# Optimization experiments

Measured on AMD Instinct MI355X. Metric: run time of the kernel, lower is better.

Reference implementation:

```python
import jax, jax.numpy as jnp
import numpy as np

NUM_QUERIES = 256
NUM_NEGATIVES = 512
NUM_GENERALIZED = 8
GEN_RADIUS = 1.0
TEMP = 0.5
STRONG_THRESHOLD = 0.97


def _mls(mu0, mu1, s0, s1):
    # mutual likelihood score; mu's are L2-normalized (F.normalize, eps=1e-12)
    mu0 = mu0 / jnp.maximum(jnp.linalg.norm(mu0, axis=-1, keepdims=True), 1e-12)
    mu1 = mu1 / jnp.maximum(jnp.linalg.norm(mu1, axis=-1, keepdims=True), 1e-12)
    down = s0 + s1
    return -0.5 * (((mu0 - mu1) ** 2) / down + jnp.log(down)).mean(-1)


def setup_inputs() -> dict:
    key = jax.random.key(0)
    B, S, H, W, C = 4, 19, 128, 128, 256
    ks = jax.random.split(key, 6)
    mu = jax.random.normal(ks[0], (B, C, H, W), jnp.float32)
    sigma = jax.random.uniform(ks[1], (B, C, H, W), jnp.float32, minval=0.1, maxval=1.0)
    cls = jax.random.randint(ks[2], (B, H, W), 0, S)
    label = jnp.transpose(jax.nn.one_hot(cls, S, dtype=jnp.float32), (0, 3, 1, 2))  # [B,S,H,W]
    mask = jnp.ones((B, 1, H, W), jnp.float32)
    prob = jax.random.uniform(ks[3], (B, S, H, W), jnp.float32)
    mmt_prototype_mu = jax.random.normal(ks[4], (S, 1, C), jnp.float32)
    mmt_prototype_sigma = jax.random.uniform(ks[5], (S, 1, C), jnp.float32, minval=0.1, maxval=1.0)
    return {"mu": mu, "sigma": sigma, "label": label, "mask": mask, "prob": prob,
            "mmt_prototype_mu": mmt_prototype_mu, "mmt_prototype_sigma": mmt_prototype_sigma,
            "epoch": 0, "iter_i": 0}


def reference(mu, sigma, label, mask, prob, mmt_prototype_mu, mmt_prototype_sigma, epoch, iter_i):
    B, C, H, W = mu.shape
    S = label.shape[1]
    P = B * H * W
    Q, NEG, G = NUM_QUERIES, NUM_NEGATIVES, NUM_GENERALIZED
    key = jax.random.key(1234)

    valid = (label * mask).transpose(1, 0, 2, 3).reshape(S, P)            # [S,P] float
    mu_f = mu.transpose(0, 2, 3, 1).reshape(P, C)                          # [P,C]
    sg_f = sigma.transpose(0, 2, 3, 1).reshape(P, C)
    prob_f = prob.transpose(1, 0, 2, 3).reshape(S, P)
    hard = (prob_f < STRONG_THRESHOLD).astype(valid.dtype) * valid         # [S,P]

    # --- segment prototypes (precision-weighted fusion), detached as in torch.no_grad ---
    inv_sg = 1.0 / sg_f
    proto_sigma_b = 1.0 / jnp.einsum('sp,pc->sc', valid, inv_sg)           # [S,C]
    proto_mu_b = proto_sigma_b * jnp.einsum('sp,pc->sc', valid, inv_sg * mu_f)
    mmt_mu = mmt_prototype_mu[:, 0, :]
    mmt_sg = mmt_prototype_sigma[:, 0, :]
    proto_sigma = 1.0 / (1.0 / proto_sigma_b + 1.0 / mmt_sg)               # momentum fusion
    proto_mu = proto_sigma * (mmt_mu / mmt_sg + proto_mu_b / proto_sigma_b)
    proto_mu = jax.lax.stop_gradient(proto_mu)
    proto_sigma = jax.lax.stop_gradient(proto_sigma)

    # cumulative masks for uniform sampling over valid / hard pixels via searchsorted
    valid_cum = jnp.cumsum(valid, axis=1)                                  # [S,P]
    valid_cnt = valid_cum[:, -1]
    hard_cum = jnp.cumsum(hard, axis=1)
    hard_cnt = hard_cum[:, -1]

    loss = jnp.float32(0.0)
    for i in range(S):
        ki = jax.random.fold_in(key, i)
        k_anc, k_cls, k_neg, k_gen = jax.random.split(ki, 4)
        # anchors: uniform over hard pixels of segment i
        u = jax.random.uniform(k_anc, (Q,)) * hard_cnt[i]
        a_idx = jnp.clip(jnp.searchsorted(hard_cum[i], u, side='right'), 0, P - 1)
        anchor_mu = mu_f[a_idx]                                            # [Q,C]
        anchor_sg = sg_f[a_idx]
        # negative class distribution from prototype MLS similarity
        others = jnp.concatenate([jnp.arange(i + 1, S), jnp.arange(0, i)])  # [S-1]
        sim = _mls(proto_mu[i][None], proto_mu[others], proto_sigma[i][None], proto_sigma[others])
        logp = jax.nn.log_softmax(sim / TEMP)
        samp = jax.random.categorical(k_cls, logp, shape=(Q, NEG))          # idx into `others`
        cls_g = others[samp.reshape(-1)]                                    # [Q*NEG] global class
        # uniform pixel within each sampled class (vectorized searchsorted over classes)
        un = jax.random.uniform(k_neg, (Q * NEG,))
        idx_all = jax.vmap(lambda cs, cnt: jnp.searchsorted(cs, un * cnt, side='right'))(valid_cum, valid_cnt)
        n_idx = jnp.clip(idx_all[cls_g, jnp.arange(Q * NEG)], 0, P - 1)
        neg_mu = jax.lax.stop_gradient(mu_f[n_idx].reshape(Q, NEG, C))
        neg_sg = jax.lax.stop_gradient(sg_f[n_idx].reshape(Q, NEG, C))
        pos_mu = jnp.broadcast_to(proto_mu[i][None, None], (Q, 1, C))
        pos_sg = jnp.broadcast_to(proto_sigma[i][None, None], (Q, 1, C))
        # generalized negatives: reparameterized samples from (updated) momentum prototypes
        eps = jax.random.normal(k_gen, (S - 1, G, C))
        gen = proto_mu[others][:, None, :] + GEN_RADIUS * jnp.sqrt(proto_sigma[others])[:, None, :] * eps
        gen = jnp.broadcast_to(gen.reshape(1, (S - 1) * G, C), (Q, (S - 1) * G, C))
        all_mu = jnp.concatenate([pos_mu, neg_mu, gen], axis=1)             # [Q,1+NEG+(S-1)*G,C]
        all_sg = jnp.concatenate([pos_sg, neg_sg, jnp.zeros_like(gen)], axis=1)
        logits = _mls(anchor_mu[:, None, :], all_mu, anchor_sg[:, None, :], all_sg) / TEMP
        loss = loss - jax.nn.log_softmax(logits, axis=-1)[:, 0].mean()      # CE vs target 0
    return loss / S
```

## Files before the change

### kernel.cpp

```cpp
#include <hip/hip_runtime.h>
#include <hip/hip_fp16.h>
#include <hip/hip_fp8.h>
#include <cstdint>

#define B_   4
#define S_   19
#define HW_  16384
#define P_   65536
#define C_   256
#define Q_   256
#define NEG_ 512
#define NS_  131072
#define GENV_ 144
#define NANCH (S_ * Q_)
#define NPAIR (NANCH / 2)
#define NBUCK 8

typedef float v2f __attribute__((ext_vector_type(2)));

#if __has_builtin(__builtin_amdgcn_cvt_pk_f32_fp8) && __has_builtin(__builtin_amdgcn_cvt_pk_fp8_f32)
#define HAVE_HW_FP8 1
#endif

template<int W> __device__ __forceinline__ v2f cvt8(uint32_t d) {
#ifdef HAVE_HW_FP8
  v2f r = __builtin_amdgcn_cvt_pk_f32_fp8((int)d, W);
  return r;
#else
  __hip_fp8_e4m3 h0, h1;
  h0.__x = (uint8_t)(d >> (W * 16));
  h1.__x = (uint8_t)(d >> (W * 16 + 8));
  v2f r; r.x = (float)h0; r.y = (float)h1; return r;
#endif
}
template<int W> __device__ __forceinline__ uint32_t pk8(float a, float b, uint32_t old) {
#ifdef HAVE_HW_FP8
  return (uint32_t)__builtin_amdgcn_cvt_pk_fp8_f32(a, b, (int)old, W);
#else
  __hip_fp8_e4m3 ha(a), hb(b);
  uint32_t v = (uint32_t)ha.__x | ((uint32_t)hb.__x << 8);
  return (old & (W ? 0x0000FFFFu : 0xFFFF0000u)) | (v << (W * 16));
#endif
}

__device__ __forceinline__ void tf2x32(uint32_t k0, uint32_t k1, uint32_t x0, uint32_t x1,
                                       uint32_t& o0, uint32_t& o1) {
  uint32_t k2 = k0 ^ k1 ^ 0x1BD11BDAu;
#define TFR(r) { x0 += x1; x1 = (x1 << r) | (x1 >> (32 - r)); x1 ^= x0; }
  x0 += k0; x1 += k1;
  TFR(13) TFR(15) TFR(26) TFR(6)  x0 += k1; x1 += k2 + 1u;
  TFR(17) TFR(29) TFR(16) TFR(24) x0 += k2; x1 += k0 + 2u;
  TFR(13) TFR(15) TFR(26) TFR(6)  x0 += k0; x1 += k1 + 3u;
  TFR(17) TFR(29) TFR(16) TFR(24) x0 += k1; x1 += k2 + 4u;
  TFR(13) TFR(15) TFR(26) TFR(6)  x0 += k2; x1 += k0 + 5u;
#undef TFR
  o0 = x0; o1 = x1;
}

__device__ __forceinline__ uint32_t rbits(uint32_t k0, uint32_t k1, uint32_t n) {
  uint32_t a, b; tf2x32(k0, k1, 0u, n, a, b); return a ^ b;
}

__device__ __forceinline__ float bits2f01(uint32_t b) {
  return __uint_as_float((b >> 9) | 0x3f800000u) - 1.0f;
}

__device__ __forceinline__ float fastrcp(float x) {
  float r; asm("v_rcp_f32 %0, %1" : "=v"(r) : "v"(x)); return r;
}

__device__ __forceinline__ float wred(float v) {
#pragma unroll
  for (int off = 32; off > 0; off >>= 1) v += __shfl_xor(v, off, 64);
  return v;
}
__device__ __forceinline__ void wred3(float& a, float& b, float& c) {
#pragma unroll
  for (int off = 32; off > 0; off >>= 1) {
    a += __shfl_xor(a, off, 64);
    b += __shfl_xor(b, off, 64);
    c += __shfl_xor(c, off, 64);
  }
}

__device__ __forceinline__ void lse_up(float lg, float& m, float& l) {
  if (lg > m) { l = l * __expf(m - lg) + 1.0f; m = lg; }
  else l += __expf(lg - m);
}
__device__ __forceinline__ void lse_merge(float& m, float& l, float mo, float lo) {
  float mn = fmaxf(m, mo);
  l = l * __expf(m - mn) + lo * __expf(mo - mn);
  m = mn;
}

__device__ __forceinline__ float erfinv_f(float x) {
  float w = -__logf(fmaxf(fmaf(-x, x, 1.0f), 1e-37f));
  float p;
  if (w < 5.0f) {
    w -= 2.5f;
    p = 2.81022636e-08f;
    p = fmaf(p, w, 3.43273939e-07f);
    p = fmaf(p, w, -3.5233877e-06f);
    p = fmaf(p, w, -4.39150654e-06f);
    p = fmaf(p, w, 0.00021858087f);
    p = fmaf(p, w, -0.00125372503f);
    p = fmaf(p, w, -0.00417768164f);
    p = fmaf(p, w, 0.246640727f);
    p = fmaf(p, w, 1.50140941f);
  } else {
    w = sqrtf(w) - 3.0f;
    p = -0.000200214257f;
    p = fmaf(p, w, 0.000100950558f);
    p = fmaf(p, w, 0.00134934322f);
    p = fmaf(p, w, -0.00367342844f);
    p = fmaf(p, w, 0.00573950773f);
    p = fmaf(p, w, -0.0076224613f);
    p = fmaf(p, w, 0.00943887047f);
    p = fmaf(p, w, 1.00167406f);
    p = fmaf(p, w, 2.83297682f);
  }
  return p * x;
}

__global__ void k_keys(uint32_t* __restrict__ keys) {
  int i = threadIdx.x;
  if (i >= S_) return;
  uint32_t f0, f1;
  tf2x32(0u, 1234u, 0u, (uint32_t)i, f0, f1);
#pragma unroll
  for (int t = 0; t < 4; ++t) {
    uint32_t a, b;
    tf2x32(f0, f1, 0u, (uint32_t)t, a, b);
    keys[i * 8 + t * 2] = a; keys[i * 8 + t * 2 + 1] = b;
  }
}

__global__ __launch_bounds__(256) void k_classify(const float* __restrict__ label,
    const float* __restrict__ mask, const float* __restrict__ prob,
    int* __restrict__ cls, int* __restrict__ hrd) {
  int p = blockIdx.x * 256 + threadIdx.x;
  int b = p >> 14, rem = p & (HW_ - 1);
  int sp = -1;
#pragma unroll
  for (int s = 0; s < S_; ++s) {
    float l = label[((b * S_ + s) << 14) + rem];
    if (l > 0.5f) sp = s;
  }
  if (mask[(b << 14) + rem] <= 0.5f) sp = -1;
  int h = 0;
  if (sp >= 0) h = (prob[((b * S_ + sp) << 14) + rem] < 0.97f) ? 1 : 0;
  cls[p] = sp; hrd[p] = h;
}

__global__ __launch_bounds__(256) void k_pack(const float* __restrict__ mu,
    const float* __restrict__ sg, uint32_t* __restrict__ pair8, float* __restrict__ norm2) {
  __shared__ float smu[64][65];
  __shared__ float ssg[64][65];
  int p0 = blockIdx.x * 64, c0 = blockIdx.y * 64;
  int b = p0 >> 14, rem0 = p0 & (HW_ - 1);
  int px = threadIdx.x & 63, cy = threadIdx.x >> 6;
#pragma unroll
  for (int itr = 0; itr < 16; ++itr) {
    int cl = cy + itr * 4;
    int addr = ((b * C_ + c0 + cl) << 14) + rem0 + px;
    smu[cl][px] = mu[addr];
    ssg[cl][px] = sg[addr];
  }
  __syncthreads();
#pragma unroll
  for (int itr = 0; itr < 8; ++itr) {
    int e = itr * 256 + threadIdx.x;
    int pxl = e >> 5, dw = e & 31, cl = dw * 2;
    uint32_t wd = pk8<0>(smu[cl][pxl], ssg[cl][pxl], 0u);
    wd = pk8<1>(smu[cl + 1][pxl], ssg[cl + 1][pxl], wd);
    pair8[(size_t)(p0 + pxl) * 128 + (c0 >> 1) + dw] = wd;
  }
  int pxn = threadIdx.x >> 2, qn = threadIdx.x & 3;
  float s2 = 0.f;
#pragma unroll
  for (int k = 0; k < 16; ++k) { float v = smu[qn * 16 + k][pxn]; s2 = fmaf(v, v, s2); }
  s2 += __shfl_xor(s2, 1, 64);
  s2 += __shfl_xor(s2, 2, 64);
  if (qn == 0) atomicAdd(&norm2[p0 + pxn], s2);
}

__global__ __launch_bounds__(256) void k_count(const int* __restrict__ cls, const int* __restrict__ hrd,
    int* __restrict__ bcv, int* __restrict__ bch) {
  __shared__ int hv[S_], hh[S_];
  int t = threadIdx.x;
  if (t < S_) { hv[t] = 0; hh[t] = 0; }
  __syncthreads();
  int p = blockIdx.x * 256 + t;
  int s = cls[p];
  if (s >= 0) { atomicAdd(&hv[s], 1); if (hrd[p]) atomicAdd(&hh[s], 1); }
  __syncthreads();
  if (t < S_) { bcv[t * 256 + blockIdx.x] = hv[t]; bch[t * 256 + blockIdx.x] = hh[t]; }
}

__global__ __launch_bounds__(320) void k_scan(const int* __restrict__ bcv, const int* __restrict__ bch,
    int* __restrict__ bov, int* __restrict__ boh,
    int* __restrict__ cntv, int* __restrict__ cnth,
    int* __restrict__ basev, int* __restrict__ baseh) {
  __shared__ int psv[S_][16], psh[S_][16], scv[S_], sch[S_];
  int t = threadIdx.x;
  int s = t >> 4, c = t & 15;
  if (t < 304) {
    int sv = 0, sh = 0;
#pragma unroll 4
    for (int b = 0; b < 16; ++b) {
      sv += bcv[s * 256 + c * 16 + b];
      sh += bch[s * 256 + c * 16 + b];
    }
    psv[s][c] = sv; psh[s][c] = sh;
  }
  __syncthreads();
  if (t < S_) {
    int rv = 0, rh = 0;
#pragma unroll
    for (int cc = 0; cc < 16; ++cc) {
      int tv = psv[t][cc]; psv[t][cc] = rv; rv += tv;
      int th = psh[t][cc]; psh[t][cc] = rh; rh += th;
    }
    cntv[t] = rv; cnth[t] = rh; scv[t] = rv; sch[t] = rh;
  }
  __syncthreads();
  if (t == 0) {
    int bv = 0, bh = 0;
    for (int k = 0; k < S_; ++k) { basev[k] = bv; bv += scv[k]; baseh[k] = bh; bh += sch[k]; }
  }
  if (t < 304) {
    int rv = psv[s][c], rh = psh[s][c];
#pragma unroll 4
    for (int b = 0; b < 16; ++b) {
      int i0 = s * 256 + c * 16 + b;
      int tv = bcv[i0]; bov[i0] = rv; rv += tv;
      int th = bch[i0]; boh[i0] = rh; rh += th;
    }
  }
}

__global__ __launch_bounds__(256) void k_fill(const int* __restrict__ cls, const int* __restrict__ hrd,
    const int* __restrict__ bov, const int* __restrict__ boh,
    const int* __restrict__ basev, const int* __restrict__ baseh,
    int* __restrict__ posv, int* __restrict__ posh) {
  __shared__ int lc[256], lh[256];
  int t = threadIdx.x;
  int p = blockIdx.x * 256 + t;
  int s = cls[p]; int h = hrd[p];
  lc[t] = s; lh[t] = h;
  __syncthreads();
  if (s >= 0) {
    int rv = 0, rh = 0;
    for (int k = 0; k < t; ++k) { if (lc[k] == s) { rv++; rh += lh[k]; } }
    posv[basev[s] + bov[s * 256 + blockIdx.x] + rv] = p;
    if (h) posh[baseh[s] + boh[s * 256 + blockIdx.x] + rh] = p;
  }
}

__global__ __launch_bounds__(256) void k_sums(const uint32_t* __restrict__ pair8,
    const int* __restrict__ cls, float* __restrict__ part) {
  __shared__ float lacc[S_][2][C_];
  __shared__ int scls[256];
  int t = threadIdx.x;
  for (int e = t; e < S_ * 2 * C_; e += 256) (&lacc[0][0][0])[e] = 0.f;
  int p0 = blockIdx.x * 256;
  scls[t] = cls[p0 + t];
  __syncthreads();
  int half = t & 1, dwi = t >> 1;
  uint32_t d = pair8[(size_t)p0 * 128 + dwi];
  for (int pp = 0; pp < 256; ++pp) {
    uint32_t dnx = (pp + 1 < 256) ? pair8[(size_t)(p0 + pp + 1) * 128 + dwi] : 0u;
    int s = scls[pp];
    if (s >= 0) {
      v2f e = half ? cvt8<1>(d) : cvt8<0>(d);
      float ia = fastrcp(e.y);
      lacc[s][0][t] += ia;
      lacc[s][1][t] += ia * e.x;
    }
    d = dnx;
  }
  __syncthreads();
  float* dst = part + (size_t)blockIdx.x * (2 * S_ * C_);
  for (int e = t; e < S_ * 2 * C_; e += 256) dst[e] = (&lacc[0][0][0])[e];
}

__global__ __launch_bounds__(256) void k_proto(const float* __restrict__ part,
    const float* __restrict__ mmu, const float* __restrict__ msg,
    float* __restrict__ pmu, float* __restrict__ psig, float* __restrict__ phat) {
  int s = blockIdx.x, c = threadIdx.x;
  float A = 0.f, Bv = 0.f;
  for (int b = 0; b < 256; ++b) {
    const float* pb = part + (size_t)b * (2 * S_ * C_) + (s * 2) * C_;
    A += pb[c];
    Bv += pb[C_ + c];
  }
  int e = s * C_ + c;
  float psb = 1.0f / A;
  float pmb = psb * Bv;
  float ms = msg[e], mm = mmu[e];
  float ps = 1.0f / (1.0f / psb + 1.0f / ms);
  float pm = ps * (mm / ms + pmb / psb);
  pmu[e] = pm; psig[e] = ps;
  __shared__ float red[4];
  float w = wred(pm * pm);
  int lane = c & 63, wv = c >> 6;
  if (lane == 0) red[wv] = w;
  __syncthreads();
  float tot = red[0] + red[1] + red[2] + red[3];
  float nrm = fmaxf(sqrtf(tot), 1e-12f);
  phat[e] = pm / nrm;
}

__global__ __launch_bounds__(64) void k_simlogp(const float* __restrict__ phat,
    const float* __restrict__ psig, float* __restrict__ logp) {
  int i = blockIdx.x, lane = threadIdx.x;
  int c0 = lane * 4;
  float phi[4], psi[4];
#pragma unroll
  for (int k = 0; k < 4; ++k) { phi[k] = phat[i * C_ + c0 + k]; psi[k] = psig[i * C_ + c0 + k]; }
  float xs[18];
#pragma unroll
  for (int j = 0; j < 18; ++j) {
    int o = i + 1 + j; if (o >= S_) o -= S_;
    float t = 0.f;
#pragma unroll
    for (int k = 0; k < 4; ++k) {
      float d = phi[k] - phat[o * C_ + c0 + k];
      float dn = psi[k] + psig[o * C_ + c0 + k];
      t += d * d / dn + logf(dn);
    }
    t = wred(t);
    xs[j] = (-0.5f * t * (1.0f / 256.0f)) * 2.0f;
  }
  float m = xs[0];
#pragma unroll
  for (int j = 1; j < 18; ++j) m = fmaxf(m, xs[j]);
  float se = 0.f;
#pragma unroll
  for (int j = 0; j < 18; ++j) se += expf(xs[j] - m);
  float lg = logf(se);
  if (lane == 0) {
#pragma unroll
    for (int j = 0; j < 18; ++j) logp[i * 18 + j] = xs[j] - m - lg;
  }
}

__global__ __launch_bounds__(256) void k_anchors(const uint32_t* __restrict__ keys,
    const int* __restrict__ cnth, const int* __restrict__ baseh,
    const int* __restrict__ posh, int* __restrict__ aidx) {
  int i = blockIdx.x, q = threadIdx.x;
  uint32_t k0 = keys[i * 8 + 0], k1 = keys[i * 8 + 1];
  float u = bits2f01(rbits(k0, k1, (uint32_t)q));
  int cnt = cnth[i];
  int idx = P_ - 1;
  if (cnt > 0) {
    int kk = (int)(u * (float)cnt);
    if (kk >= cnt) kk = cnt - 1;
    idx = posh[baseh[i] + kk];
  }
  aidx[i * Q_ + q] = idx;
}

__global__ __launch_bounds__(256) void k_gen(const uint32_t* __restrict__ keys,
    const float* __restrict__ pmu, const float* __restrict__ psig, float* __restrict__ ghat) {
  int v = blockIdx.x, i = blockIdx.y, c = threadIdx.x;
  int o = i + 1 + (v >> 3); if (o >= S_) o -= S_;
  uint32_t k0 = keys[i * 8 + 6], k1 = keys[i * 8 + 7];
  uint32_t bits = rbits(k0, k1, (uint32_t)(v * C_ + c));
  float f01 = bits2f01(bits);
  const float lo = -0.99999994f;
  float u = fmaxf(f01 * 2.0f + lo, lo);
  float eps = 1.41421356237f * erfinv_f(u);
  float g = pmu[o * C_ + c] + sqrtf(psig[o * C_ + c]) * eps;
  __shared__ float red[4];
  float w = wred(g * g);
  int lane = c & 63, wv = c >> 6;
  if (lane == 0) red[wv] = w;
  __syncthreads();
  float tot = red[0] + red[1] + red[2] + red[3];
  float nrm = fmaxf(sqrtf(tot), 1e-12f);
  ghat[((size_t)(i * GENV_ + v)) * C_ + c] = g / nrm;
}

__global__ __launch_bounds__(256) void k_sample(const uint32_t* __restrict__ keys,
    const float* __restrict__ logp, const int* __restrict__ cntv, const int* __restrict__ basev,
    const int* __restrict__ posv, int* __restrict__ nidx) {
  int i = blockIdx.y;
  int m = blockIdx.x * 256 + threadIdx.x;
  __shared__ float lp[18];
  __shared__ int lcnt[S_], lbase[S_];
  int t = threadIdx.x;
  if (t < 18) lp[t] = logp[i * 18 + t];
  if (t < S_) { lcnt[t] = cntv[t]; lbase[t] = basev[t]; }
  __syncthreads();
  uint32_t kc0 = keys[i * 8 + 2], kc1 = keys[i * 8 + 3];
  uint32_t kn0 = keys[i * 8 + 4], kn1 = keys[i * 8 + 5];
  float bv = -1e30f; int best = 0;
  for (int s = 0; s < 18; ++s) {
    uint32_t b = rbits(kc0, kc1, (uint32_t)m * 18u + (uint32_t)s);
    float u = fmaxf(bits2f01(b), 1.17549435e-38f);
    float g = -__logf(-__logf(u)) + lp[s];
    if (g > bv) { bv = g; best = s; }
  }
  float un = bits2f01(rbits(kn0, kn1, (uint32_t)m));
  int cc = i + 1 + best; if (cc >= S_) cc -= S_;
  int cnt = lcnt[cc];
  int idx = P_ - 1;
  if (cnt > 0) {
    int kk = (int)(un * (float)cnt);
    if (kk >= cnt) kk = cnt - 1;
    idx = posv[lbase[cc] + kk];
  }
  nidx[(size_t)i * NS_ + m] = idx;
}

__global__ __launch_bounds__(64) void k_bucket(const int* __restrict__ nidx,
    int* __restrict__ snidx, int* __restrict__ boff) {
  int a = blockIdx.x;
  int lane = threadIdx.x;
  const int* src = nidx + (size_t)a * NEG_;
  int e[8], bk[8];
#pragma unroll
  for (int c = 0; c < 8; ++c) { e[c] = src[c * 64 + lane]; bk[c] = (e[c] >> 13) & 7; }
  uint32_t cnt[NBUCK];
#pragma unroll
  for (int b = 0; b < NBUCK; ++b) cnt[b] = 0;
#pragma unroll
  for (int c = 0; c < 8; ++c)
#pragma unroll
    for (int b = 0; b < NBUCK; ++b) {
      unsigned long long mb = __ballot(bk[c] == b);
      cnt[b] += (uint32_t)__popcll(mb);
    }
  uint32_t base[NBUCK]; uint32_t run = 0;
#pragma unroll
  for (int b = 0; b < NBUCK; ++b) { base[b] = run; run += cnt[b]; }
  if (lane < NBUCK) boff[a * 9 + lane] = (int)base[lane];
  if (lane == 0) boff[a * 9 + 8] = NEG_;
  uint32_t off[NBUCK];
#pragma unroll
  for (int b = 0; b < NBUCK; ++b) off[b] = 0;
  unsigned long long ltm = (1ull << lane) - 1ull;
#pragma unroll
  for (int c = 0; c < 8; ++c) {
    int pos = 0;
#pragma unroll
    for (int b = 0; b < NBUCK; ++b) {
      unsigned long long mb = __ballot(bk[c] == b);
      if (bk[c] == b) pos = (int)(base[b] + off[b] + (uint32_t)__popcll(mb & ltm));
      off[b] += (uint32_t)__popcll(mb);
    }
    snidx[(size_t)a * NEG_ + pos] = e[c];
  }
}

__global__ __launch_bounds__(64) void k_neg(const uint32_t* __restrict__ pair8,
    const float* __restrict__ norm2, const int* __restrict__ snidx,
    const int* __restrict__ boff, const int* __restrict__ aidx,
    float2* __restrict__ partial) {
  __shared__ float4 anc[260];
  __shared__ float4 ah2s[130];
  int bid = blockIdx.x;
  int bucket = bid & 7;
  int pr = bid >> 3;
  int a0 = pr * 2, a1 = a0 + 1;
  int lane = threadIdx.x;

  int ap0 = aidx[a0], ap1 = aidx[a1];
  float rn0 = fastrcp(fmaxf(sqrtf(norm2[ap0]), 1e-12f));
  float rn1 = fastrcp(fmaxf(sqrtf(norm2[ap1]), 1e-12f));
  uint2 d0 = ((const uint2*)(pair8 + (size_t)ap0 * 128))[lane];
  uint2 d1 = ((const uint2*)(pair8 + (size_t)ap1 * 128))[lane];
  {
    v2f ex = cvt8<0>(d0.x), ey = cvt8<1>(d0.x), ez = cvt8<0>(d0.y), ew = cvt8<1>(d0.y);
    float h0 = ex.x * rn0, h1 = ey.x * rn0, h2 = ez.x * rn0, h3 = ew.x * rn0;
    anc[lane * 2]     = make_float4(h0, ex.y, h1, ey.y);
    anc[lane * 2 + 1] = make_float4(h2, ez.y, h3, ew.y);
    ah2s[lane]        = make_float4(h0 * h0, h1 * h1, h2 * h2, h3 * h3);
    ex = cvt8<0>(d1.x); ey = cvt8<1>(d1.x); ez = cvt8<0>(d1.y); ew = cvt8<1>(d1.y);
    h0 = ex.x * rn1; h1 = ey.x * rn1; h2 = ez.x * rn1; h3 = ew.x * rn1;
    anc[130 + lane * 2]     = make_float4(h0, ex.y, h1, ey.y);
    anc[130 + lane * 2 + 1] = make_float4(h2, ez.y, h3, ew.y);
    ah2s[65 + lane]         = make_float4(h0 * h0, h1 * h1, h2 * h2, h3 * h3);
  }
  __syncthreads();

  int s0 = boff[a0 * 9 + bucket], e0i = boff[a0 * 9 + bucket + 1];
  int s1 = boff[a1 * 9 + bucket], e1i = boff[a1 * 9 + bucket + 1];
  int L0 = e0i - s0, L1 = e1i - s1, Lt = L0 + L1;
  const int* list0 = snidx + (size_t)a0 * NEG_ + s0;
  const int* list1 = snidx + (size_t)a1 * NEG_ + s1;

  float m0 = -1e30f, l0 = 0.f, m1 = -1e30f, l1 = 0.f;

  for (int r = 0; r * 64 < Lt; ++r) {
    int g = r * 64 + lane;
    bool act = g < Lt;
    int which = (act && g >= L0) ? 1 : 0;
    int j = which ? (g - L0) : g;
    int p = act ? (which ? list1[j] : list0[j]) : ap0;
    float rnN = fastrcp(fmaxf(sqrtf(norm2[p]), 1e-12f));
    const uint4* rp = (const uint4*)(pair8 + (size_t)p * 128);
    const float4* A = anc + which * 130;
    const float4* H = ah2s + which * 65;
    float sA = 0.f, sC = 0.f, sNR = 0.f, sL = 0.f;
    uint4 c0 = rp[0], c1 = rp[1];
#pragma unroll 1
    for (int it = 0; it < 16; ++it) {
      int nx = ((it + 1) & 15) * 2;
      uint4 n0 = rp[nx], n1 = rp[nx + 1];
      uint32_t dws[8] = {c0.x, c0.y, c0.z, c0.w, c1.x, c1.y, c1.z, c1.w};
      float pp = 1.0f, pq = 1.0f;
#pragma unroll
      for (int gq = 0; gq < 4; ++gq) {
        float4 acA = A[it * 8 + gq * 2];
        float4 acB = A[it * 8 + gq * 2 + 1];
        float4 hh = H[it * 4 + gq];
        v2f e0v = cvt8<0>(dws[2 * gq]),     e1v = cvt8<1>(dws[2 * gq]);
        v2f e2v = cvt8<0>(dws[2 * gq + 1]), e3v = cvt8<1>(dws[2 * gq + 1]);
        float dn0 = acA.y + e0v.y, dn1 = acA.w + e1v.y;
        float dn2 = acB.y + e2v.y, dn3 = acB.w + e3v.y;
        float d01 = dn0 * dn1, d23 = dn2 * dn3;
        float R01 = fastrcp(d01), R23 = fastrcp(d23);
        pp *= d01; pq *= d23;
        float r0 = dn1 * R01, r1 = dn0 * R01, r2 = dn3 * R23, r3 = dn2 * R23;
        sA = fmaf(hh.x, r0, sA); sA = fmaf(hh.y, r1, sA);
        sA = fmaf(hh.z, r2, sA); sA = fmaf(hh.w, r3, sA);
        float q0 = e0v.x * r0; sC = fmaf(acA.x, q0, sC); sNR = fmaf(e0v.x, q0, sNR);
        float q1 = e1v.x * r1; sC = fmaf(acA.z, q1, sC); sNR = fmaf(e1v.x, q1, sNR);
        float q2 = e2v.x * r2; sC = fmaf(acB.x, q2, sC); sNR = fmaf(e2v.x, q2, sNR);
        float q3 = e3v.x * r3; sC = fmaf(acB.z, q3, sC); sNR = fmaf(e3v.x, q3, sNR);
      }
      sL += __logf(pp * pq);
      c0 = n0; c1 = n1;
    }
    float tt = sA + rnN * rnN * sNR - 2.0f * rnN * sC + sL;
    float lg = -tt * (1.0f / 256.0f);
    if (act) { if (which) lse_up(lg, m1, l1); else lse_up(lg, m0, l0); }
  }
#pragma unroll
  for (int o = 32; o > 0; o >>= 1) {
    float mo = __shfl_xor(m0, o, 64), lo = __shfl_xor(l0, o, 64);
    lse_merge(m0, l0, mo, lo);
    mo = __shfl_xor(m1, o, 64); lo = __shfl_xor(l1, o, 64);
    lse_merge(m1, l1, mo, lo);
  }
  if (lane == 0) {
    partial[a0 * NBUCK + bucket] = make_float2(m0, l0);
    partial[a1 * NBUCK + bucket] = make_float2(m1, l1);
  }
}

__global__ __launch_bounds__(256, 4) void k_fin(const uint32_t* __restrict__ pair8,
    const float* __restrict__ norm2,
    const float* __restrict__ phat, const float* __restrict__ psig,
    const float* __restrict__ ghat, const int* __restrict__ aidx,
    const float2* __restrict__ partial, float* __restrict__ out) {
  __shared__ float2 ancG[C_];
  __shared__ float redm[3][4];
  __shared__ float2 mlw[4];

  int bid = blockIdx.x;
  int i = bid >> 8;
  int t = threadIdx.x, w = t >> 6, lane = t & 63;

  int ap = aidx[bid];
  uint32_t ad = pair8[(size_t)ap * 128 + (t >> 1)];
  v2f ae0 = cvt8<0>(ad), ae1 = cvt8<1>(ad);
  float amu = (t & 1) ? ae1.x : ae0.x;
  float asg = (t & 1) ? ae1.y : ae0.y;
  float rn = fastrcp(fmaxf(sqrtf(norm2[ap]), 1e-12f));
  float ahat = amu * rn;
  float wv = fastrcp(asg);
  ancG[t] = make_float2(wv, ahat * wv);

  float pm = phat[i * C_ + t];
  float ps = psig[i * C_ + t];
  float dnp = asg + ps;
  float dd = ahat - pm;
  float post = fmaf(dd * dd, fastrcp(dnp), __logf(dnp));
  float a1t = ahat * ahat * wv;
  float lat = __logf(asg);
  wred3(post, a1t, lat);
  if (lane == 0) { redm[0][w] = post; redm[1][w] = a1t; redm[2][w] = lat; }
  __syncthreads();
  float postS = redm[0][0] + redm[0][1] + redm[0][2] + redm[0][3];
  float Kc = (redm[1][0] + redm[1][1] + redm[1][2] + redm[1][3])
           + (redm[2][0] + redm[2][1] + redm[2][2] + redm[2][3]);
  float logit0 = -postS * (1.0f / 256.0f);

  float m = -1e30f, l = 0.0f;
  const float4* ancGf = (const float4*)ancG;
  if (lane < 36) {
    int g = lane * 4 + w;
    const float4* gp = (const float4*)(ghat + ((size_t)(i * GENV_ + g)) * C_);
    float a1 = 0.f, a2 = 0.f;
    for (int itr = 0; itr < 64; ++itr) {
      float4 gv = gp[itr];
      float4 g01 = ancGf[itr * 2];
      float4 g23 = ancGf[itr * 2 + 1];
      a1 = fmaf(gv.x * gv.x, g01.x, a1); a2 = fmaf(gv.x, g01.y, a2);
      a1 = fmaf(gv.y * gv.y, g01.z, a1); a2 = fmaf(gv.y, g01.w, a2);
      a1 = fmaf(gv.z * gv.z, g23.x, a1); a2 = fmaf(gv.z, g23.y, a2);
      a1 = fmaf(gv.w * gv.w, g23.z, a1); a2 = fmaf(gv.w, g23.w, a2);
    }
    float lg = -(Kc + a1 - 2.0f * a2) * (1.0f / 256.0f);
    lse_up(lg, m, l);
  }
#pragma unroll
  for (int o = 32; o > 0; o >>= 1) {
    float mo = __shfl_xor(m, o, 64);
    float lo = __shfl_xor(l, o, 64);
    lse_merge(m, l, mo, lo);
  }
  if (lane == 0) mlw[w] = make_float2(m, l);
  __syncthreads();
  if (t == 0) {
    float mm = mlw[0].x, ll = mlw[0].y;
    lse_merge(mm, ll, mlw[1].x, mlw[1].y);
    lse_merge(mm, ll, mlw[2].x, mlw[2].y);
    lse_merge(mm, ll, mlw[3].x, mlw[3].y);
    const float2* pp = partial + (size_t)bid * NBUCK;
#pragma unroll
    for (int b = 0; b < NBUCK; ++b) lse_merge(mm, ll, pp[b].x, pp[b].y);
    lse_merge(mm, ll, logit0, 1.0f);
    float lse = mm + __logf(ll);
    float contrib = logit0 - lse;
    atomicAdd(out, -contrib * (1.0f / (19.0f * 256.0f)));
  }
}

extern "C" void kernel_launch(void* const* d_in, const int* in_sizes, int n_in,
                              void* d_out, int out_size, void* d_ws, size_t ws_size,
                              hipStream_t stream) {
  const float* mu    = (const float*)d_in[0];
  const float* sg    = (const float*)d_in[1];
  const float* label = (const float*)d_in[2];
  const float* mask  = (const float*)d_in[3];
  const float* prob  = (const float*)d_in[4];
  const float* mmu   = (const float*)d_in[5];
  const float* msg   = (const float*)d_in[6];

  char* ws = (char*)d_ws;
  size_t off = 0;
  auto take = [&](size_t bytes) { size_t r = off; off = (off + bytes + 255) & ~(size_t)255; return r; };
  size_t o_pair8 = take((size_t)P_ * 128 * 4);
  size_t o_norm2 = take((size_t)P_ * 4);
  size_t o_cls   = take((size_t)P_ * 4);
  size_t o_hrd   = take((size_t)P_ * 4);
  size_t o_bcv   = take(S_ * 256 * 4);
  size_t o_bch   = take(S_ * 256 * 4);
  size_t o_bov   = take(S_ * 256 * 4);
  size_t o_boh   = take(S_ * 256 * 4);
  size_t o_cntv  = take(S_ * 4);
  size_t o_cnth  = take(S_ * 4);
  size_t o_basev = take(S_ * 4);
  size_t o_baseh = take(S_ * 4);
  size_t o_posv  = take((size_t)P_ * 4);
  size_t o_posh  = take((size_t)P_ * 4);
  size_t o_part  = take((size_t)256 * 2 * S_ * C_ * 4);
  size_t o_pmu   = take(S_ * C_ * 4);
  size_t o_psig  = take(S_ * C_ * 4);
  size_t o_phat  = take(S_ * C_ * 4);
  size_t o_logp  = take(S_ * 18 * 4);
  size_t o_keys  = take(S_ * 8 * 4);
  size_t o_aidx  = take(S_ * Q_ * 4);
  size_t o_nidx  = take((size_t)S_ * NS_ * 4);
  size_t o_snidx = take((size_t)S_ * NS_ * 4);
  size_t o_boff  = take((size_t)NANCH * 9 * 4);
  size_t o_lpar  = take((size_t)NANCH * NBUCK * 8);
  size_t o_ghat  = take((size_t)S_ * GENV_ * C_ * 4);
  if (ws_size < off) return;

  uint32_t* pair8 = (uint32_t*)(ws + o_pair8);
  float*    norm2 = (float*)(ws + o_norm2);
  int*      cls   = (int*)(ws + o_cls);
  int*      hrd   = (int*)(ws + o_hrd);
  int*      bcv   = (int*)(ws + o_bcv);
  int*      bch   = (int*)(ws + o_bch);
  int*      bov   = (int*)(ws + o_bov);
  int*      boh   = (int*)(ws + o_boh);
  int*      cntv  = (int*)(ws + o_cntv);
  int*      cnth  = (int*)(ws + o_cnth);
  int*      basev = (int*)(ws + o_basev);
  int*      baseh = (int*)(ws + o_baseh);
  int*      posv  = (int*)(ws + o_posv);
  int*      posh  = (int*)(ws + o_posh);
  float*    part  = (float*)(ws + o_part);
  float*    pmu   = (float*)(ws + o_pmu);
  float*    psig  = (float*)(ws + o_psig);
  float*    phat  = (float*)(ws + o_phat);
  float*    logp  = (float*)(ws + o_logp);
  uint32_t* keys  = (uint32_t*)(ws + o_keys);
  int*      aidx  = (int*)(ws + o_aidx);
  int*      nidx  = (int*)(ws + o_nidx);
  int*      snidx = (int*)(ws + o_snidx);
  int*      boff  = (int*)(ws + o_boff);
  float2*   lpar  = (float2*)(ws + o_lpar);
  float*    ghat  = (float*)(ws + o_ghat);

  hipMemsetAsync(ws + o_norm2, 0, (size_t)P_ * 4, stream);
  hipMemsetAsync(d_out, 0, (size_t)out_size * 4, stream);

  k_keys<<<1, 64, 0, stream>>>(keys);
  k_classify<<<256, 256, 0, stream>>>(label, mask, prob, cls, hrd);
  k_pack<<<dim3(P_ / 64, C_ / 64), 256, 0, stream>>>(mu, sg, pair8, norm2);
  k_count<<<256, 256, 0, stream>>>(cls, hrd, bcv, bch);
  k_scan<<<1, 320, 0, stream>>>(bcv, bch, bov, boh, cntv, cnth, basev, baseh);
  k_fill<<<256, 256, 0, stream>>>(cls, hrd, bov, boh, basev, baseh, posv, posh);
  k_sums<<<256, 256, 0, stream>>>(pair8, cls, part);
  k_proto<<<S_, 256, 0, stream>>>(part, mmu, msg, pmu, psig, phat);
  k_simlogp<<<S_, 64, 0, stream>>>(phat, psig, logp);
  k_anchors<<<S_, 256, 0, stream>>>(keys, cnth, baseh, posh, aidx);
  k_gen<<<dim3(GENV_, S_), 256, 0, stream>>>(keys, pmu, psig, ghat);
  k_sample<<<dim3(512, S_), 256, 0, stream>>>(keys, logp, cntv, basev, posv, nidx);
  k_bucket<<<NANCH, 64, 0, stream>>>(nidx, snidx, boff);
  k_neg<<<NBUCK * NPAIR, 64, 0, stream>>>(pair8, norm2, snidx, boff, aidx, lpar);
  k_fin<<<NANCH, 256, 0, stream>>>(pair8, norm2, phat, psig, ghat, aidx, lpar, (float*)d_out);
}
```

Before: 657.9 us.

## Split fp8 pair rows into separate mu and sigma halves for packed math

Changes the packed fp8 row layout from interleaved (mu,sigma) pairs to a mu half followed by a sigma half, so each dword holds four channels of one quantity. k_neg keeps the anchor in three separate shared arrays and does the per-channel MLS math with 2-wide vector ops (a macro), aiming for packed FP32 instructions and fewer conversions per dword. k_pack switches to float4 global loads, and k_sums/k_fin are updated to the new layout. The risk is more shared-memory reads per iteration, and k_sums loses its software prefetch.

```diff
diff --git a/kernel.cpp b/kernel.cpp
--- a/kernel.cpp
+++ b/kernel.cpp
@@ -12,7 +12,7 @@
 #define NEG_ 512
 #define NS_  131072
 #define GENV_ 144
-#define NANCH (S_ * Q_)
+#define NANCH (S_ * 256)
 #define NPAIR (NANCH / 2)
 #define NBUCK 8
 
@@ -158,22 +158,31 @@
   __shared__ float ssg[64][65];
   int p0 = blockIdx.x * 64, c0 = blockIdx.y * 64;
   int b = p0 >> 14, rem0 = p0 & (HW_ - 1);
-  int px = threadIdx.x & 63, cy = threadIdx.x >> 6;
-#pragma unroll
-  for (int itr = 0; itr < 16; ++itr) {
-    int cl = cy + itr * 4;
-    int addr = ((b * C_ + c0 + cl) << 14) + rem0 + px;
-    smu[cl][px] = mu[addr];
-    ssg[cl][px] = sg[addr];
-  }
-  __syncthreads();
-#pragma unroll
-  for (int itr = 0; itr < 8; ++itr) {
+  int cl0 = threadIdx.x >> 4, px4 = (threadIdx.x & 15) * 4;
+#pragma unroll
+  for (int itr = 0; itr < 4; ++itr) {
+    int cl = cl0 + itr * 16;
+    int addr = ((b * C_ + c0 + cl) << 14) + rem0 + px4;
+    float4 vm = *reinterpret_cast<const float4*>(mu + addr);
+    float4 vs = *reinterpret_cast<const float4*>(sg + addr);
+    smu[cl][px4 + 0] = vm.x; smu[cl][px4 + 1] = vm.y;
+    smu[cl][px4 + 2] = vm.z; smu[cl][px4 + 3] = vm.w;
+    ssg[cl][px4 + 0] = vs.x; ssg[cl][px4 + 1] = vs.y;
+    ssg[cl][px4 + 2] = vs.z; ssg[cl][px4 + 3] = vs.w;
+  }
+  __syncthreads();
+#pragma unroll
+  for (int itr = 0; itr < 4; ++itr) {
     int e = itr * 256 + threadIdx.x;
-    int pxl = e >> 5, dw = e & 31, cl = dw * 2;
-    uint32_t wd = pk8<0>(smu[cl][pxl], ssg[cl][pxl], 0u);
-    wd = pk8<1>(smu[cl + 1][pxl], ssg[cl + 1][pxl], wd);
-    pair8[(size_t)(p0 + pxl) * 128 + (c0 >> 1) + dw] = wd;
+    int pxl = e >> 4, dq = e & 15;
+    int cb = dq * 4;
+    uint32_t wm = pk8<0>(smu[cb][pxl], smu[cb + 1][pxl], 0u);
+    wm = pk8<1>(smu[cb + 2][pxl], smu[cb + 3][pxl], wm);
+    uint32_t wsv = pk8<0>(ssg[cb][pxl], ssg[cb + 1][pxl], 0u);
+    wsv = pk8<1>(ssg[cb + 2][pxl], ssg[cb + 3][pxl], wsv);
+    size_t rowb = (size_t)(p0 + pxl) * 128;
+    pair8[rowb + (c0 >> 2) + dq] = wm;
+    pair8[rowb + 64 + (c0 >> 2) + dq] = wsv;
   }
   int pxn = threadIdx.x >> 2, qn = threadIdx.x & 3;
   float s2 = 0.f;
@@ -266,18 +275,21 @@
   int p0 = blockIdx.x * 256;
   scls[t] = cls[p0 + t];
   __syncthreads();
-  int half = t & 1, dwi = t >> 1;
-  uint32_t d = pair8[(size_t)p0 * 128 + dwi];
+  int dq = t >> 2, sub = t & 3;
   for (int pp = 0; pp < 256; ++pp) {
-    uint32_t dnx = (pp + 1 < 256) ? pair8[(size_t)(p0 + pp + 1) * 128 + dwi] : 0u;
     int s = scls[pp];
+    size_t rowb = (size_t)(p0 + pp) * 128;
+    uint32_t dm = pair8[rowb + dq];
+    uint32_t dsv = pair8[rowb + 64 + dq];
     if (s >= 0) {
-      v2f e = half ? cvt8<1>(d) : cvt8<0>(d);
-      float ia = fastrcp(e.y);
+      v2f em = (sub & 2) ? cvt8<1>(dm) : cvt8<0>(dm);
+      v2f es = (sub & 2) ? cvt8<1>(dsv) : cvt8<0>(dsv);
+      float mv = (sub & 1) ? em.y : em.x;
+      float sv = (sub & 1) ? es.y : es.x;
+      float ia = fastrcp(sv);
       lacc[s][0][t] += ia;
-      lacc[s][1][t] += ia * e.x;
-    }
-    d = dnx;
+      lacc[s][1][t] += ia * mv;
+    }
   }
   __syncthreads();
   float* dst = part + (size_t)blockIdx.x * (2 * S_ * C_);
@@ -454,12 +466,35 @@
   }
 }
 
+#define PKQ(DM, DS, QI) {                                         \
+    float4 ah4 = AH[QI]; float4 as4 = AS[QI]; float4 h24 = H2[QI];\
+    v2f m01 = cvt8<0>(DM), m23 = cvt8<1>(DM);                     \
+    v2f g01 = cvt8<0>(DS), g23 = cvt8<1>(DS);                     \
+    v2f asA; asA.x = as4.x; asA.y = as4.y;                        \
+    v2f asB; asB.x = as4.z; asB.y = as4.w;                        \
+    v2f dA = asA + g01;                                           \
+    v2f dB = asB + g23;                                           \
+    float dpA = dA.x * dA.y, dpB = dB.x * dB.y;                   \
+    float RA = fastrcp(dpA), RB = fastrcp(dpB);                   \
+    pp *= dpA * dpB;                                              \
+    v2f rA; rA.x = dA.y * RA; rA.y = dA.x * RA;                   \
+    v2f rB; rB.x = dB.y * RB; rB.y = dB.x * RB;                   \
+    v2f h2A; h2A.x = h24.x; h2A.y = h24.y;                        \
+    v2f h2B; h2B.x = h24.z; h2B.y = h24.w;                        \
+    sAv += h2A * rA; sAv += h2B * rB;                             \
+    v2f qA = m01 * rA, qB = m23 * rB;                             \
+    v2f ahA; ahA.x = ah4.x; ahA.y = ah4.y;                        \
+    v2f ahB; ahB.x = ah4.z; ahB.y = ah4.w;                        \
+    sCv += ahA * qA; sCv += ahB * qB;                             \
+    sNRv += m01 * qA; sNRv += m23 * qB; }
+
 __global__ __launch_bounds__(64) void k_neg(const uint32_t* __restrict__ pair8,
     const float* __restrict__ norm2, const int* __restrict__ snidx,
     const int* __restrict__ boff, const int* __restrict__ aidx,
     float2* __restrict__ partial) {
-  __shared__ float4 anc[260];
-  __shared__ float4 ah2s[130];
+  __shared__ float4 ahP[2][66];
+  __shared__ float4 asP[2][66];
+  __shared__ float4 h2P[2][66];
   int bid = blockIdx.x;
   int bucket = bid & 7;
   int pr = bid >> 3;
@@ -469,19 +504,23 @@
   int ap0 = aidx[a0], ap1 = aidx[a1];
   float rn0 = fastrcp(fmaxf(sqrtf(norm2[ap0]), 1e-12f));
   float rn1 = fastrcp(fmaxf(sqrtf(norm2[ap1]), 1e-12f));
-  uint2 d0 = ((const uint2*)(pair8 + (size_t)ap0 * 128))[lane];
-  uint2 d1 = ((const uint2*)(pair8 + (size_t)ap1 * 128))[lane];
   {
-    v2f ex = cvt8<0>(d0.x), ey = cvt8<1>(d0.x), ez = cvt8<0>(d0.y), ew = cvt8<1>(d0.y);
-    float h0 = ex.x * rn0, h1 = ey.x * rn0, h2 = ez.x * rn0, h3 = ew.x * rn0;
-    anc[lane * 2]     = make_float4(h0, ex.y, h1, ey.y);
-    anc[lane * 2 + 1] = make_float4(h2, ez.y, h3, ew.y);
-    ah2s[lane]        = make_float4(h0 * h0, h1 * h1, h2 * h2, h3 * h3);
-    ex = cvt8<0>(d1.x); ey = cvt8<1>(d1.x); ez = cvt8<0>(d1.y); ew = cvt8<1>(d1.y);
-    h0 = ex.x * rn1; h1 = ey.x * rn1; h2 = ez.x * rn1; h3 = ew.x * rn1;
-    anc[130 + lane * 2]     = make_float4(h0, ex.y, h1, ey.y);
-    anc[130 + lane * 2 + 1] = make_float4(h2, ez.y, h3, ew.y);
-    ah2s[65 + lane]         = make_float4(h0 * h0, h1 * h1, h2 * h2, h3 * h3);
+    const uint32_t* r0 = pair8 + (size_t)ap0 * 128;
+    uint32_t dm = r0[lane], dsv = r0[64 + lane];
+    v2f m01 = cvt8<0>(dm), m23 = cvt8<1>(dm);
+    v2f s01 = cvt8<0>(dsv), s23 = cvt8<1>(dsv);
+    float h0 = m01.x * rn0, h1 = m01.y * rn0, h2 = m23.x * rn0, h3 = m23.y * rn0;
+    ahP[0][lane] = make_float4(h0, h1, h2, h3);
+    asP[0][lane] = make_float4(s01.x, s01.y, s23.x, s23.y);
+    h2P[0][lane] = make_float4(h0 * h0, h1 * h1, h2 * h2, h3 * h3);
+    const uint32_t* r1 = pair8 + (size_t)ap1 * 128;
+    dm = r1[lane]; dsv = r1[64 + lane];
+    m01 = cvt8<0>(dm); m23 = cvt8<1>(dm);
+    s01 = cvt8<0>(dsv); s23 = cvt8<1>(dsv);
+    h0 = m01.x * rn1; h1 = m01.y * rn1; h2 = m23.x * rn1; h3 = m23.y * rn1;
+    ahP[1][lane] = make_float4(h0, h1, h2, h3);
+    asP[1][lane] = make_float4(s01.x, s01.y, s23.x, s23.y);
+    h2P[1][lane] = make_float4(h0 * h0, h1 * h1, h2 * h2, h3 * h3);
   }
   __syncthreads();
 
@@ -500,40 +539,27 @@
     int j = which ? (g - L0) : g;
     int p = act ? (which ? list1[j] : list0[j]) : ap0;
     float rnN = fastrcp(fmaxf(sqrtf(norm2[p]), 1e-12f));
-    const uint4* rp = (const uint4*)(pair8 + (size_t)p * 128);
-    const float4* A = anc + which * 130;
-    const float4* H = ah2s + which * 65;
-    float sA = 0.f, sC = 0.f, sNR = 0.f, sL = 0.f;
-    uint4 c0 = rp[0], c1 = rp[1];
+    const uint4* rm = (const uint4*)(pair8 + (size_t)p * 128);
+    const uint4* rs = rm + 16;
+    const float4* AH = ahP[which];
+    const float4* AS = asP[which];
+    const float4* H2 = h2P[which];
+    v2f sAv = {0.f, 0.f}, sCv = {0.f, 0.f}, sNRv = {0.f, 0.f};
+    float sL = 0.f;
+    uint4 cm = rm[0], cs = rs[0];
 #pragma unroll 1
     for (int it = 0; it < 16; ++it) {
-      int nx = ((it + 1) & 15) * 2;
-      uint4 n0 = rp[nx], n1 = rp[nx + 1];
-      uint32_t dws[8] = {c0.x, c0.y, c0.z, c0.w, c1.x, c1.y, c1.z, c1.w};
-      float pp = 1.0f, pq = 1.0f;
-#pragma unroll
-      for (int gq = 0; gq < 4; ++gq) {
-        float4 acA = A[it * 8 + gq * 2];
-        float4 acB = A[it * 8 + gq * 2 + 1];
-        float4 hh = H[it * 4 + gq];
-        v2f e0v = cvt8<0>(dws[2 * gq]),     e1v = cvt8<1>(dws[2 * gq]);
-        v2f e2v = cvt8<0>(dws[2 * gq + 1]), e3v = cvt8<1>(dws[2 * gq + 1]);
-        float dn0 = acA.y + e0v.y, dn1 = acA.w + e1v.y;
-        float dn2 = acB.y + e2v.y, dn3 = acB.w + e3v.y;
-        float d01 = dn0 * dn1, d23 = dn2 * dn3;
-        float R01 = fastrcp(d01), R23 = fastrcp(d23);
-        pp *= d01; pq *= d23;
-        float r0 = dn1 * R01, r1 = dn0 * R01, r2 = dn3 * R23, r3 = dn2 * R23;
-        sA = fmaf(hh.x, r0, sA); sA = fmaf(hh.y, r1, sA);
-        sA = fmaf(hh.z, r2, sA); sA = fmaf(hh.w, r3, sA);
-        float q0 = e0v.x * r0; sC = fmaf(acA.x, q0, sC); sNR = fmaf(e0v.x, q0, sNR);
-        float q1 = e1v.x * r1; sC = fmaf(acA.z, q1, sC); sNR = fmaf(e1v.x, q1, sNR);
-        float q2 = e2v.x * r2; sC = fmaf(acB.x, q2, sC); sNR = fmaf(e2v.x, q2, sNR);
-        float q3 = e3v.x * r3; sC = fmaf(acB.z, q3, sC); sNR = fmaf(e3v.x, q3, sNR);
-      }
-      sL += __logf(pp * pq);
-      c0 = n0; c1 = n1;
-    }
+      int nx = (it + 1) & 15;
+      uint4 nmv = rm[nx], nsv = rs[nx];
+      float pp = 1.0f;
+      PKQ(cm.x, cs.x, it * 4 + 0)
+      PKQ(cm.y, cs.y, it * 4 + 1)
+      PKQ(cm.z, cs.z, it * 4 + 2)
+      PKQ(cm.w, cs.w, it * 4 + 3)
+      sL += __logf(pp);
+      cm = nmv; cs = nsv;
+    }
+    float sA = sAv.x + sAv.y, sC = sCv.x + sCv.y, sNR = sNRv.x + sNRv.y;
     float tt = sA + rnN * rnN * sNR - 2.0f * rnN * sC + sL;
     float lg = -tt * (1.0f / 256.0f);
     if (act) { if (which) lse_up(lg, m1, l1); else lse_up(lg, m0, l0); }
@@ -565,10 +591,12 @@
   int t = threadIdx.x, w = t >> 6, lane = t & 63;
 
   int ap = aidx[bid];
-  uint32_t ad = pair8[(size_t)ap * 128 + (t >> 1)];
-  v2f ae0 = cvt8<0>(ad), ae1 = cvt8<1>(ad);
-  float amu = (t & 1) ? ae1.x : ae0.x;
-  float asg = (t & 1) ? ae1.y : ae0.y;
+  uint32_t dm = pair8[(size_t)ap * 128 + (t >> 2)];
+  uint32_t dsg = pair8[(size_t)ap * 128 + 64 + (t >> 2)];
+  v2f em = (t & 2) ? cvt8<1>(dm) : cvt8<0>(dm);
+  v2f es = (t & 2) ? cvt8<1>(dsg) : cvt8<0>(dsg);
+  float amu = (t & 1) ? em.y : em.x;
+  float asg = (t & 1) ? es.y : es.x;
   float rn = fastrcp(fmaxf(sqrtf(norm2[ap]), 1e-12f));
   float ahat = amu * rn;
   float wv = fastrcp(asg);
```

Measured after the change: 777.0 us. 1.18x slower.
